# Optimization experiments

Hardware: AMD Instinct MI355X
Metric: run time of the kernel (lower is better)

Reference implementation:

```python
import jax, jax.numpy as jnp
import numpy as np

B, T, D = 64, 512, 128          # batch, time, input_dim
S = 16                           # num_sessions
P, STRIDE = 3, 1                 # patch size / stride
H = 512                          # hidden_size
HORIZONS = (1, 5, 10)
K = len(HORIZONS)
TOK = D * P                      # token_dim = 384
EPS = 1e-6


def setup_inputs() -> dict:
    key = jax.random.key(0)
    ks = jax.random.split(key, 16)
    s = 0.02
    return {
        "x": jax.random.normal(ks[0], (B, T, D), jnp.float32),
        "session_idx": jax.random.randint(ks[1], (B,), 0, S),
        # per-session affine (expert) params
        "sess_W": jax.random.normal(ks[2], (S, D, D), jnp.float32) * s,
        "sess_b": jax.random.normal(ks[3], (S, D), jnp.float32) * s,
        # projection token_dim -> hidden
        "proj_W": jax.random.normal(ks[4], (H, TOK), jnp.float32) * s,
        "proj_b": jax.random.normal(ks[5], (H,), jnp.float32) * s,
        "rms_scale": jnp.ones((H,), jnp.float32),
        # single-layer GRU params (PyTorch layout: [3H, in], gate order r,z,n)
        "gru_Wih": jax.random.normal(ks[6], (3 * H, H), jnp.float32) * s,
        "gru_Whh": jax.random.normal(ks[7], (3 * H, H), jnp.float32) * s,
        "gru_bih": jax.random.normal(ks[8], (3 * H,), jnp.float32) * s,
        "gru_bhh": jax.random.normal(ks[9], (3 * H,), jnp.float32) * s,
        # future heads (K horizons): Linear(H,H) -> GELU -> Linear(H,TOK)
        "head_W1": jax.random.normal(ks[10], (K, H, H), jnp.float32) * s,
        "head_b1": jax.random.normal(ks[11], (K, H), jnp.float32) * s,
        "head_W2": jax.random.normal(ks[12], (K, TOK, H), jnp.float32) * s,
        "head_b2": jax.random.normal(ks[13], (K, TOK), jnp.float32) * s,
    }


def _forward(x, session_idx, sess_W, sess_b, proj_W, proj_b, rms_scale,
             gru_Wih, gru_Whh, gru_bih, gru_bhh,
             head_W1, head_b1, head_W2, head_b2):
    # --- per-sample session affine (expert gather + batched GEMM) ---
    W = sess_W[session_idx]                      # [B, D, D]
    b = sess_b[session_idx]                      # [B, D]
    aligned = jnp.einsum('btd,bed->bte', x, W) + b[:, None, :]  # y = x @ W.T + b

    # --- patch unfold along time; torch unfold gives [N, D, P] -> flatten (d,p) ---
    N = (T - P) // STRIDE + 1
    idx = jnp.arange(N)[:, None] * STRIDE + jnp.arange(P)[None, :]  # [N, P]
    win = aligned[:, idx, :]                     # [B, N, P, D]
    tokens = jnp.transpose(win, (0, 1, 3, 2)).reshape(B, N, TOK)    # [B, N, D*P]

    # --- projection + RMSNorm ---
    h = tokens @ proj_W.T + proj_b               # [B, N, H]
    rms = jnp.sqrt(jnp.mean(h * h, axis=-1, keepdims=True) + EPS)
    h = h / rms * rms_scale

    # --- GRU (PyTorch gate order r, z, n) via lax.scan over time ---
    gx = h @ gru_Wih.T + gru_bih                 # [B, N, 3H], precomputed input gates
    gx_t = jnp.transpose(gx, (1, 0, 2))          # [N, B, 3H]

    def step(hprev, g):
        gh = hprev @ gru_Whh.T + gru_bhh         # [B, 3H]
        r = jax.nn.sigmoid(g[:, :H] + gh[:, :H])
        z = jax.nn.sigmoid(g[:, H:2 * H] + gh[:, H:2 * H])
        n = jnp.tanh(g[:, 2 * H:] + r * gh[:, 2 * H:])
        hn = (1.0 - z) * n + z * hprev
        return hn, hn

    h0 = jnp.zeros((B, H), h.dtype)
    _, hs = jax.lax.scan(step, h0, gx_t)         # [N, B, H]
    hidden = jnp.transpose(hs, (1, 0, 2))        # [B, N, H]

    # --- multi-head future MLPs (stacked over K horizons) ---
    a = jnp.einsum('bnh,kfh->kbnf', hidden, head_W1) + head_b1[:, None, None, :]
    a = jax.nn.gelu(a, approximate=False)        # torch nn.GELU default = exact
    preds = jnp.einsum('kbnf,ktf->kbnt', a, head_W2) + head_b2[:, None, None, :]
    return preds, tokens                          # preds: [K, B, N, TOK]


def reference(x, session_idx, sess_W, sess_b, proj_W, proj_b, rms_scale,
              gru_Wih, gru_Whh, gru_bih, gru_bhh,
              head_W1, head_b1, head_W2, head_b2):
    return _forward(x, session_idx, sess_W, sess_b, proj_W, proj_b, rms_scale,
                    gru_Wih, gru_Whh, gru_bih, gru_bhh,
                    head_W1, head_b1, head_W2, head_b2)
```

## Files before the change

### kernel.cpp

```cpp
#include <hip/hip_runtime.h>
#include <hip/hip_bf16.h>
#include <math.h>

typedef __hip_bfloat16 bf16;
typedef __attribute__((ext_vector_type(8))) short short8;
typedef __attribute__((ext_vector_type(4))) short short4v;
typedef __attribute__((ext_vector_type(4))) float f32x4;

#define B_    64
#define T_    512
#define D_    128
#define N_    510
#define H_    512
#define TOK_  384
#define PRED1_ 12533760L
#define TOKOFF_ 37601280L

#define O_XBF  0UL
#define O_SWB  8388608UL
#define O_PW   8912896UL
#define O_WIH  9306112UL
#define O_WHH  10878976UL
#define O_W1   12451840UL
#define O_W2   14024704UL
#define O_TOK  15204352UL
#define O_HBF  40271872UL
#define O_HID  73695232UL
#define O_ABF  107118592UL
#define O_GX   140541952UL

__global__ void k_f2b(const float* __restrict__ s, bf16* __restrict__ d, int n4) {
  int i = blockIdx.x * 256 + threadIdx.x;
  if (i < n4) {
    float4 v = ((const float4*)s)[i];
    union { short4v sv; bf16 h[4]; } u;
    u.h[0] = __float2bfloat16(v.x); u.h[1] = __float2bfloat16(v.y);
    u.h[2] = __float2bfloat16(v.z); u.h[3] = __float2bfloat16(v.w);
    ((short4v*)d)[i] = u.sv;
  }
}

enum { EPI_F32 = 0, EPI_BF16 = 1, EPI_GELU = 2, EPI_TOK = 3, EPI_F32R = 4 };
#define SLDA 40

template <int EPI>
__global__ __launch_bounds__(256, 2) void k_gemm(
    const bf16* __restrict__ A, const bf16* __restrict__ W,
    const float* __restrict__ bias, void* __restrict__ C,
    int K, int ldc, long zA, long zW, long zB, long zC,
    const int* __restrict__ sidx, float* __restrict__ tokf, bf16* __restrict__ tokb)
{
  const int tid = threadIdx.x;
  const int bm = blockIdx.x, bn = blockIdx.y, z = blockIdx.z;
  const int wsel = (EPI == EPI_TOK) ? sidx[z] : z;
  const int lane = tid & 63, wave = tid >> 6;
  const int wm = (wave & 1) << 6, wn = (wave >> 1) << 6;
  const int r16 = lane & 15, quad = lane >> 4;

  __shared__ bf16 sA[128 * SLDA];
  __shared__ bf16 sB[128 * SLDA];

  const bf16* Ag = A + (long)z * zA + (long)bm * 128 * K;
  const bf16* Wg = W + (long)wsel * zW + (long)bn * 128 * K;

  f32x4 zf = {0.f, 0.f, 0.f, 0.f};
  f32x4 acc[4][4];
  for (int i = 0; i < 4; ++i) for (int j = 0; j < 4; ++j) acc[i][j] = zf;

  const int sr = tid >> 1, sc = (tid & 1) << 4;
  for (int k0 = 0; k0 < K; k0 += 32) {
    *(short8*)&sA[sr*SLDA + sc]     = *(const short8*)&Ag[(long)sr*K + k0 + sc];
    *(short8*)&sA[sr*SLDA + sc + 8] = *(const short8*)&Ag[(long)sr*K + k0 + sc + 8];
    *(short8*)&sB[sr*SLDA + sc]     = *(const short8*)&Wg[(long)sr*K + k0 + sc];
    *(short8*)&sB[sr*SLDA + sc + 8] = *(const short8*)&Wg[(long)sr*K + k0 + sc + 8];
    __syncthreads();
    short8 fa[4], fb[4];
    for (int i = 0; i < 4; ++i) fa[i] = *(const short8*)&sA[(wm + i*16 + r16)*SLDA + quad*8];
    for (int j = 0; j < 4; ++j) fb[j] = *(const short8*)&sB[(wn + j*16 + r16)*SLDA + quad*8];
    for (int i = 0; i < 4; ++i)
      for (int j = 0; j < 4; ++j)
        acc[i][j] = __builtin_amdgcn_mfma_f32_16x16x32_bf16(fa[i], fb[j], acc[i][j], 0, 0, 0);
    __syncthreads();
  }

  const float* bz = bias + (long)wsel * zB + bn * 128;
  for (int i = 0; i < 4; ++i) {
    for (int j = 0; j < 4; ++j) {
      const int colL = wn + j*16 + r16;
      const float bv = bz[colL];
      for (int r = 0; r < 4; ++r) {
        float v = acc[i][j][r] + bv;
        const long grow = (long)bm*128 + wm + i*16 + quad*4 + r;
        const long gcol = (long)bn*128 + colL;
        if (EPI == EPI_F32) {
          ((float*)C)[(long)z*zC + grow*ldc + gcol] = v;
        } else if (EPI == EPI_BF16) {
          ((bf16*)C)[(long)z*zC + grow*ldc + gcol] = __float2bfloat16(v);
        } else if (EPI == EPI_GELU) {
          v = 0.5f * v * (1.0f + erff(v * 0.70710678118654752f));
          ((bf16*)C)[(long)z*zC + grow*ldc + gcol] = __float2bfloat16(v);
        } else if (EPI == EPI_F32R) {
          const long rb = grow & 63, rn = grow >> 6;
          ((float*)C)[(rb*510 + rn)*ldc + gcol] = v;
        } else {
          for (int p = 0; p < 3; ++p) {
            long n = grow - p;
            if (n >= 0 && n < N_) {
              tokf[((long)z*N_ + n)*TOK_ + gcol*3 + p] = v;
              tokb[((long)n*B_ + z)*TOK_ + gcol*3 + p] = __float2bfloat16(v);
            }
          }
        }
      }
    }
  }
}

__global__ __launch_bounds__(256) void k_rms(const float* __restrict__ hpre,
                                             const float* __restrict__ scale,
                                             bf16* __restrict__ hbf)
{
  const int wave = threadIdx.x >> 6, lane = threadIdx.x & 63;
  const long row = (long)blockIdx.x * 4 + wave;
  const float* p = hpre + row * 512 + lane * 8;
  float4 v0 = *(const float4*)p;
  float4 v1 = *(const float4*)(p + 4);
  float ss = v0.x*v0.x + v0.y*v0.y + v0.z*v0.z + v0.w*v0.w
           + v1.x*v1.x + v1.y*v1.y + v1.z*v1.z + v1.w*v1.w;
  for (int m = 32; m >= 1; m >>= 1) ss += __shfl_xor(ss, m, 64);
  const float inv = 1.0f / sqrtf(ss * (1.0f/512.0f) + 1e-6f);
  const float* sc = scale + lane * 8;
  union { short8 sv; bf16 h[8]; } u;
  u.h[0] = __float2bfloat16(v0.x*inv*sc[0]); u.h[1] = __float2bfloat16(v0.y*inv*sc[1]);
  u.h[2] = __float2bfloat16(v0.z*inv*sc[2]); u.h[3] = __float2bfloat16(v0.w*inv*sc[3]);
  u.h[4] = __float2bfloat16(v1.x*inv*sc[4]); u.h[5] = __float2bfloat16(v1.y*inv*sc[5]);
  u.h[6] = __float2bfloat16(v1.z*inv*sc[6]); u.h[7] = __float2bfloat16(v1.w*inv*sc[7]);
  *(short8*)(hbf + row * 512 + lane * 8) = u.sv;
}

#define KP 520

#define GL2LDS(g, l) __builtin_amdgcn_global_load_lds( \
    (const __attribute__((address_space(1))) void*)(g), \
    (__attribute__((address_space(3))) void*)(l), 16, 0, 16)

__global__ __launch_bounds__(192, 1) void k_gru(
    const bf16* __restrict__ gx,
    const bf16* __restrict__ Whh,
    const float* __restrict__ bhh,
    bf16* __restrict__ hidden,
    int* __restrict__ flags)
{
  const int tid = threadIdx.x;
  const int g = tid / 64;
  const int lane = tid & 63;
  const int c16 = lane & 15, quad = lane >> 4;
  const int cw = blockIdx.x & 31;
  const int gb = blockIdx.x >> 5;
  const int hw = cw * 16;
  const int b0 = gb * 8;

  __shared__ bf16 hp[16 * KP];
  __shared__ float ex[2][16 * 16];

  short8 wf[16];
  {
    const bf16* wrow = Whh + (long)(g*512 + hw + c16) * 512;
    for (int kt = 0; kt < 16; ++kt) wf[kt] = *(const short8*)&wrow[kt*32 + quad*8];
  }
  const float bh = bhh[g*512 + hw + c16];

  {
    short8 z8 = {0,0,0,0,0,0,0,0};
    for (int c = tid; c < 16*KP/8; c += 192) *(short8*)&hp[c*8] = z8;
  }
  __syncthreads();

  int* myflag = &flags[(gb*32 + cw) * 32];
  const int pidx = (gb*32 + (lane & 31)) * 32;

  const int brv = (quad & 1) * 4;

  float gxv[4], gxn[4];
  {
    const bf16* gxs = gx + (long)b0 * 1536 + g*512 + hw + c16;
    for (int i2 = 0; i2 < 4; ++i2)
      gxv[i2] = __bfloat162float(gxs[(long)(brv + i2) * 1536]);
  }

  for (int s = 0; s < 510; ++s) {
    {
      const int s1 = (s < 509) ? s + 1 : 509;
      const bf16* gxs = gx + ((long)s1*64 + b0)*1536 + g*512 + hw + c16;
      for (int i2 = 0; i2 < 4; ++i2)
        gxn[i2] = __bfloat162float(gxs[(long)(brv + i2) * 1536]);
    }
    if (s > 0) {
      while (true) {
        int v = __hip_atomic_load(&flags[pidx], __ATOMIC_RELAXED, __HIP_MEMORY_SCOPE_AGENT);
        if (__all(v >= s)) break;
        __builtin_amdgcn_s_sleep(1);
      }
      asm volatile("" ::: "memory");
      const bf16* src = hidden + ((long)(s-1)*64 + b0)*512 + lane*8;
      for (int b = g; b < 8; b += 3) {
        GL2LDS(src + b*512, &hp[b*KP]);
      }
    }
    __syncthreads();

    f32x4 acc = {0.f,0.f,0.f,0.f};
    for (int kt = 0; kt < 16; ++kt) {
      short8 a = *(const short8*)&hp[c16*KP + kt*32 + quad*8];
      acc = __builtin_amdgcn_mfma_f32_16x16x32_bf16(a, wf[kt], acc, 0, 0, 0);
    }

    if (g < 2) {
      for (int i2 = 0; i2 < 4; ++i2) {
        float pre = gxv[i2] + acc[i2] + bh;
        ex[g][(quad*4 + i2)*16 + c16] = 1.0f / (1.0f + expf(-pre));
      }
    }
    __syncthreads();
    if (g == 2) {
      if (quad < 2) {
        for (int i2 = 0; i2 < 4; ++i2) {
          const int br = quad*4 + i2;
          const float rr = ex[0][br*16 + c16];
          const float zz = ex[1][br*16 + c16];
          const float nn = tanhf(gxv[i2] + rr * (acc[i2] + bh));
          const float hpv = __bfloat162float(hp[br*KP + hw + c16]);
          const float hn = (1.0f - zz)*nn + zz*hpv;
          union { bf16 h; unsigned short u; } cb; cb.h = __float2bfloat16(hn);
          unsigned int mine = cb.u;
          unsigned int part = (unsigned int)__shfl_xor((int)mine, 1, 64);
          if (!(c16 & 1)) {
            unsigned int w = (part << 16) | mine;
            __hip_atomic_store((unsigned int*)(hidden + ((long)s*64 + b0 + br)*512 + hw + c16),
                               w, __ATOMIC_RELAXED, __HIP_MEMORY_SCOPE_AGENT);
          }
        }
      }
      if (s < 509) {
        asm volatile("s_waitcnt vmcnt(0)" ::: "memory");
        if (lane == 0)
          __hip_atomic_store(myflag, s + 1, __ATOMIC_RELAXED, __HIP_MEMORY_SCOPE_AGENT);
      }
    }
    for (int i = 0; i < 4; ++i) gxv[i] = gxn[i];
  }
}

extern "C" void kernel_launch(void* const* d_in, const int* in_sizes, int n_in,
                              void* d_out, int out_size, void* d_ws, size_t ws_size,
                              hipStream_t stream)
{
  const float* x    = (const float*)d_in[0];
  const int*   sidx = (const int*)d_in[1];
  const float* sW   = (const float*)d_in[2];
  const float* sb   = (const float*)d_in[3];
  const float* pW   = (const float*)d_in[4];
  const float* pb   = (const float*)d_in[5];
  const float* rsc  = (const float*)d_in[6];
  const float* wih  = (const float*)d_in[7];
  const float* whh  = (const float*)d_in[8];
  const float* bih  = (const float*)d_in[9];
  const float* bhh  = (const float*)d_in[10];
  const float* w1   = (const float*)d_in[11];
  const float* b1   = (const float*)d_in[12];
  const float* w2   = (const float*)d_in[13];
  const float* b2   = (const float*)d_in[14];
  char* ws = (char*)d_ws;
  float* out = (float*)d_out;

  bf16* xbf   = (bf16*)(ws + O_XBF);
  bf16* swbf  = (bf16*)(ws + O_SWB);
  bf16* pwbf  = (bf16*)(ws + O_PW);
  bf16* wihbf = (bf16*)(ws + O_WIH);
  bf16* whhbf = (bf16*)(ws + O_WHH);
  bf16* w1bf  = (bf16*)(ws + O_W1);
  bf16* w2bf  = (bf16*)(ws + O_W2);
  bf16* tokbf = (bf16*)(ws + O_TOK);
  bf16* hbf   = (bf16*)(ws + O_HBF);
  bf16* hidbf = (bf16*)(ws + O_HID);
  bf16* abf   = (bf16*)(ws + O_ABF);
  int*  bar   = (int*)(ws + O_ABF);
  float* hpre = (float*)(ws + O_GX);
  bf16* gxbf  = (bf16*)(ws + O_GX);

  auto cvt = [&](const float* s, bf16* dp, long n) {
    int n4 = (int)(n >> 2);
    k_f2b<<<dim3((n4 + 255) / 256), dim3(256), 0, stream>>>(s, dp, n4);
  };
  cvt(x,   xbf,   (long)B_*T_*D_);
  cvt(sW,  swbf,  16L*128*128);
  cvt(pW,  pwbf,  512L*384);
  cvt(wih, wihbf, 1536L*512);
  cvt(whh, whhbf, 1536L*512);
  cvt(w1,  w1bf,  3L*512*512);
  cvt(w2,  w2bf,  3L*384*512);

  k_gemm<EPI_TOK><<<dim3(4, 1, 64), dim3(256), 0, stream>>>(
      xbf, swbf, sb, nullptr, 128, 0,
      (long)T_*D_, 128L*128, 128L, 0L, sidx, out + TOKOFF_, tokbf);

  k_gemm<EPI_F32><<<dim3(255, 4, 1), dim3(256), 0, stream>>>(
      tokbf, pwbf, pb, hpre, 384, 512, 0, 0, 0, 0, nullptr, nullptr, nullptr);

  k_rms<<<dim3(8160), dim3(256), 0, stream>>>(hpre, rsc, hbf);

  k_gemm<EPI_BF16><<<dim3(255, 12, 1), dim3(256), 0, stream>>>(
      hbf, wihbf, bih, gxbf, 512, 1536, 0, 0, 0, 0, nullptr, nullptr, nullptr);

  hipMemsetAsync(ws + O_ABF, 0, 32768, stream);
  k_gru<<<dim3(256), dim3(192), 0, stream>>>(gxbf, whhbf, bhh, hidbf, bar);

  for (int k = 0; k < 3; ++k) {
    k_gemm<EPI_GELU><<<dim3(255, 4, 1), dim3(256), 0, stream>>>(
        hidbf, w1bf + (long)k*512*512, b1 + (long)k*512, abf,
        512, 512, 0, 0, 0, 0, nullptr, nullptr, nullptr);
    k_gemm<EPI_F32R><<<dim3(255, 3, 1), dim3(256), 0, stream>>>(
        abf, w2bf + (long)k*384*512, b2 + (long)k*384, out + (long)k*PRED1_,
        512, 384, 0, 0, 0, 0, nullptr, nullptr, nullptr);
  }
}
```

Baseline: 2.121 ms.

## Give each GRU wave all three gates and drop LDS staging and block barriers

The GRU recurrence is restructured so each wave owns a 16-column slice for all three gates (r, z, n). It keeps all three weight fragments in registers and loads the previous hidden state straight from global memory into MFMA operands. This removes the LDS staging, the two __syncthreads per step and the cross-wave exchange of gate activations. The launch changes from 256 blocks of 3 waves to 64 blocks of 4 waves. Each wave now publishes its own flag, which cuts intra-block synchronisation on the serial critical path, at the cost of higher register pressure (48 short8 weight fragments) and more uncoalesced per-lane global loads each step.

Result: slower. 3.761 ms (+77.3%).

```diff
diff --git a/kernel.cpp b/kernel.cpp
--- a/kernel.cpp
+++ b/kernel.cpp
@@ -138,116 +138,132 @@
   *(short8*)(hbf + row * 512 + lane * 8) = u.sv;
 }
 
-#define KP 520
-
-#define GL2LDS(g, l) __builtin_amdgcn_global_load_lds( \
-    (const __attribute__((address_space(1))) void*)(g), \
-    (__attribute__((address_space(3))) void*)(l), 16, 0, 16)
-
-__global__ __launch_bounds__(192, 1) void k_gru(
+__global__ __launch_bounds__(256, 1) void k_gru(
     const bf16* __restrict__ gx,
     const bf16* __restrict__ Whh,
     const float* __restrict__ bhh,
     bf16* __restrict__ hidden,
     int* __restrict__ flags)
 {
-  const int tid = threadIdx.x;
-  const int g = tid / 64;
+  const int tid  = threadIdx.x;
+  const int wv   = tid >> 6;
   const int lane = tid & 63;
-  const int c16 = lane & 15, quad = lane >> 4;
-  const int cw = blockIdx.x & 31;
-  const int gb = blockIdx.x >> 5;
-  const int hw = cw * 16;
-  const int b0 = gb * 8;
-
-  __shared__ bf16 hp[16 * KP];
-  __shared__ float ex[2][16 * 16];
-
-  short8 wf[16];
+  const int c16  = lane & 15, quad = lane >> 4;
+  const int wg   = blockIdx.x & 7;
+  const int gb   = blockIdx.x >> 3;
+  const int pw   = wg * 4 + wv;
+  const int hwv  = pw * 16;
+  const int b0   = gb * 8;
+
+  short8 wr[16], wz[16], wn[16];
   {
-    const bf16* wrow = Whh + (long)(g*512 + hw + c16) * 512;
-    for (int kt = 0; kt < 16; ++kt) wf[kt] = *(const short8*)&wrow[kt*32 + quad*8];
-  }
-  const float bh = bhh[g*512 + hw + c16];
-
+    const bf16* r0 = Whh + (long)(       hwv + c16) * 512;
+    const bf16* z0 = Whh + (long)( 512 + hwv + c16) * 512;
+    const bf16* n0 = Whh + (long)(1024 + hwv + c16) * 512;
+#pragma unroll
+    for (int kt = 0; kt < 16; ++kt) {
+      wr[kt] = *(const short8*)&r0[kt*32 + quad*8];
+      wz[kt] = *(const short8*)&z0[kt*32 + quad*8];
+      wn[kt] = *(const short8*)&n0[kt*32 + quad*8];
+    }
+  }
+  const float bhr = bhh[       hwv + c16];
+  const float bhz = bhh[ 512 + hwv + c16];
+  const float bhn = bhh[1024 + hwv + c16];
+
+  int* myflag = &flags[(gb*32 + pw) * 32];
+  const int pidx = (gb*32 + (lane & 31)) * 32;
+  const int brv = (quad & 1) * 4;
+
+  float gr[4], gz[4], gn[4], pr[4], pz[4], pn[4];
   {
-    short8 z8 = {0,0,0,0,0,0,0,0};
-    for (int c = tid; c < 16*KP/8; c += 192) *(short8*)&hp[c*8] = z8;
-  }
-  __syncthreads();
-
-  int* myflag = &flags[(gb*32 + cw) * 32];
-  const int pidx = (gb*32 + (lane & 31)) * 32;
-
-  const int brv = (quad & 1) * 4;
-
-  float gxv[4], gxn[4];
-  {
-    const bf16* gxs = gx + (long)b0 * 1536 + g*512 + hw + c16;
-    for (int i2 = 0; i2 < 4; ++i2)
-      gxv[i2] = __bfloat162float(gxs[(long)(brv + i2) * 1536]);
+    const bf16* gxs = gx + (long)b0 * 1536 + hwv + c16;
+#pragma unroll
+    for (int i2 = 0; i2 < 4; ++i2) {
+      const long ro = (long)(brv + i2) * 1536;
+      gr[i2] = __bfloat162float(gxs[ro]);
+      gz[i2] = __bfloat162float(gxs[ro + 512]);
+      gn[i2] = __bfloat162float(gxs[ro + 1024]);
+    }
   }
 
   for (int s = 0; s < 510; ++s) {
     {
       const int s1 = (s < 509) ? s + 1 : 509;
-      const bf16* gxs = gx + ((long)s1*64 + b0)*1536 + g*512 + hw + c16;
-      for (int i2 = 0; i2 < 4; ++i2)
-        gxn[i2] = __bfloat162float(gxs[(long)(brv + i2) * 1536]);
-    }
+      const bf16* gxs = gx + ((long)s1*64 + b0)*1536 + hwv + c16;
+#pragma unroll
+      for (int i2 = 0; i2 < 4; ++i2) {
+        const long ro = (long)(brv + i2) * 1536;
+        pr[i2] = __bfloat162float(gxs[ro]);
+        pz[i2] = __bfloat162float(gxs[ro + 512]);
+        pn[i2] = __bfloat162float(gxs[ro + 1024]);
+      }
+    }
+
+    f32x4 ar = {0.f,0.f,0.f,0.f}, az = {0.f,0.f,0.f,0.f}, an = {0.f,0.f,0.f,0.f};
+    float hpv[4] = {0.f,0.f,0.f,0.f};
+
     if (s > 0) {
       while (true) {
-        int v = __hip_atomic_load(&flags[pidx], __ATOMIC_RELAXED, __HIP_MEMORY_SCOPE_AGENT);
-        if (__all(v >= s)) break;
+        int fv = __hip_atomic_load(&flags[pidx], __ATOMIC_RELAXED, __HIP_MEMORY_SCOPE_AGENT);
+        if (__all(fv >= s)) break;
         __builtin_amdgcn_s_sleep(1);
       }
       asm volatile("" ::: "memory");
-      const bf16* src = hidden + ((long)(s-1)*64 + b0)*512 + lane*8;
-      for (int b = g; b < 8; b += 3) {
-        GL2LDS(src + b*512, &hp[b*KP]);
-      }
-    }
-    __syncthreads();
-
-    f32x4 acc = {0.f,0.f,0.f,0.f};
-    for (int kt = 0; kt < 16; ++kt) {
-      short8 a = *(const short8*)&hp[c16*KP + kt*32 + quad*8];
-      acc = __builtin_amdgcn_mfma_f32_16x16x32_bf16(a, wf[kt], acc, 0, 0, 0);
-    }
-
-    if (g < 2) {
+
+      union { unsigned long long q[2]; short8 s8; } au[16];
+      {
+        const unsigned long long* hq = (const unsigned long long*)
+            (hidden + ((long)(s-1)*64 + b0 + (c16 & 7)) * 512);
+#pragma unroll
+        for (int kt = 0; kt < 16; ++kt) {
+          au[kt].q[0] = __hip_atomic_load(hq + kt*8 + quad*2,     __ATOMIC_RELAXED, __HIP_MEMORY_SCOPE_AGENT);
+          au[kt].q[1] = __hip_atomic_load(hq + kt*8 + quad*2 + 1, __ATOMIC_RELAXED, __HIP_MEMORY_SCOPE_AGENT);
+        }
+      }
+      {
+        const unsigned* hpd = (const unsigned*)(hidden + ((long)(s-1)*64 + b0)*512);
+#pragma unroll
+        for (int i2 = 0; i2 < 4; ++i2) {
+          unsigned d = __hip_atomic_load(hpd + ((long)(brv+i2)*512 + hwv + (c16 & ~1))/2,
+                                         __ATOMIC_RELAXED, __HIP_MEMORY_SCOPE_AGENT);
+          union { unsigned short u; bf16 h; } cb;
+          cb.u = (unsigned short)((c16 & 1) ? (d >> 16) : (d & 0xffff));
+          hpv[i2] = __bfloat162float(cb.h);
+        }
+      }
+#pragma unroll
+      for (int kt = 0; kt < 16; ++kt) {
+        ar = __builtin_amdgcn_mfma_f32_16x16x32_bf16(au[kt].s8, wr[kt], ar, 0, 0, 0);
+        az = __builtin_amdgcn_mfma_f32_16x16x32_bf16(au[kt].s8, wz[kt], az, 0, 0, 0);
+        an = __builtin_amdgcn_mfma_f32_16x16x32_bf16(au[kt].s8, wn[kt], an, 0, 0, 0);
+      }
+    }
+
+    if (quad < 2) {
+#pragma unroll
       for (int i2 = 0; i2 < 4; ++i2) {
-        float pre = gxv[i2] + acc[i2] + bh;
-        ex[g][(quad*4 + i2)*16 + c16] = 1.0f / (1.0f + expf(-pre));
-      }
-    }
-    __syncthreads();
-    if (g == 2) {
-      if (quad < 2) {
-        for (int i2 = 0; i2 < 4; ++i2) {
-          const int br = quad*4 + i2;
-          const float rr = ex[0][br*16 + c16];
-          const float zz = ex[1][br*16 + c16];
-          const float nn = tanhf(gxv[i2] + rr * (acc[i2] + bh));
-          const float hpv = __bfloat162float(hp[br*KP + hw + c16]);
-          const float hn = (1.0f - zz)*nn + zz*hpv;
-          union { bf16 h; unsigned short u; } cb; cb.h = __float2bfloat16(hn);
-          unsigned int mine = cb.u;
-          unsigned int part = (unsigned int)__shfl_xor((int)mine, 1, 64);
-          if (!(c16 & 1)) {
-            unsigned int w = (part << 16) | mine;
-            __hip_atomic_store((unsigned int*)(hidden + ((long)s*64 + b0 + br)*512 + hw + c16),
-                               w, __ATOMIC_RELAXED, __HIP_MEMORY_SCOPE_AGENT);
-          }
+        const float r  = 1.0f / (1.0f + expf(-(gr[i2] + ar[i2] + bhr)));
+        const float z  = 1.0f / (1.0f + expf(-(gz[i2] + az[i2] + bhz)));
+        const float nn = tanhf(gn[i2] + r * (an[i2] + bhn));
+        const float hn = (1.0f - z)*nn + z*hpv[i2];
+        union { bf16 h; unsigned short u; } cb; cb.h = __float2bfloat16(hn);
+        unsigned mine = cb.u;
+        unsigned part = (unsigned)__shfl_xor((int)mine, 1, 64);
+        if (!(c16 & 1)) {
+          unsigned w = (part << 16) | mine;
+          __hip_atomic_store((unsigned*)(hidden + ((long)s*64 + b0 + brv + i2)*512 + hwv + c16),
+                             w, __ATOMIC_RELAXED, __HIP_MEMORY_SCOPE_AGENT);
         }
       }
-      if (s < 509) {
-        asm volatile("s_waitcnt vmcnt(0)" ::: "memory");
-        if (lane == 0)
-          __hip_atomic_store(myflag, s + 1, __ATOMIC_RELAXED, __HIP_MEMORY_SCOPE_AGENT);
-      }
-    }
-    for (int i = 0; i < 4; ++i) gxv[i] = gxn[i];
+    }
+    if (s < 509) {
+      asm volatile("s_waitcnt vmcnt(0)" ::: "memory");
+      if (lane == 0)
+        __hip_atomic_store(myflag, s + 1, __ATOMIC_RELAXED, __HIP_MEMORY_SCOPE_AGENT);
+    }
+#pragma unroll
+    for (int i2 = 0; i2 < 4; ++i2) { gr[i2]=pr[i2]; gz[i2]=pz[i2]; gn[i2]=pn[i2]; }
   }
 }
 
@@ -313,7 +329,7 @@
       hbf, wihbf, bih, gxbf, 512, 1536, 0, 0, 0, 0, nullptr, nullptr, nullptr);
 
   hipMemsetAsync(ws + O_ABF, 0, 32768, stream);
-  k_gru<<<dim3(256), dim3(192), 0, stream>>>(gxbf, whhbf, bhh, hidbf, bar);
+  k_gru<<<dim3(64), dim3(256), 0, stream>>>(gxbf, whhbf, bhh, hidbf, bar);
 
   for (int k = 0; k < 3; ++k) {
     k_gemm<EPI_GELU><<<dim3(255, 4, 1), dim3(256), 0, stream>>>(
```
